# Optimization experiments

Hardware: AMD Instinct MI355X
Metric: run time of the kernel (lower is better)

The kernel has to match this reference:

```python
import jax, jax.numpy as jnp
import numpy as np

P = 512        # number of graph pairs
MAXN = 192     # max(len_s) by construction
D_IN = 32      # num_input_features
HID = 64       # hidden_dim
REG = 0.1      # entropic reg
ITERS = 8      # numItermax in forward call
DEG = 8        # avg degree for synthetic edges


def setup_inputs() -> dict:
    key = jax.random.key(0)
    ks = jax.random.split(key, 16)
    len_s = np.asarray(96 + (np.arange(P) % 97), dtype=np.int32)          # 96..192
    len_t = np.asarray(32 + ((np.arange(P) * 7) % 65), dtype=np.int32)    # 32..96 <= len_s
    Ns, Nt = int(len_s.sum()), int(len_t.sum())
    return {
        "x_s": jax.random.normal(ks[0], (Ns, D_IN), jnp.float32),
        "x_t": jax.random.normal(ks[1], (Nt, D_IN), jnp.float32),
        "W_rel0": 0.1 * jax.random.normal(ks[2], (D_IN, HID), jnp.float32),
        "b_rel0": 0.1 * jax.random.normal(ks[3], (HID,), jnp.float32),
        "W_root0": 0.1 * jax.random.normal(ks[4], (D_IN, HID), jnp.float32),
        "W_rel1": 0.1 * jax.random.normal(ks[5], (HID, HID), jnp.float32),
        "b_rel1": 0.1 * jax.random.normal(ks[6], (HID,), jnp.float32),
        "W_root1": 0.1 * jax.random.normal(ks[7], (HID, HID), jnp.float32),
        "W_e": 0.1 * jax.random.normal(ks[8], (D_IN + 2 * HID, 64), jnp.float32),
        "b_e": 0.1 * jax.random.normal(ks[9], (64,), jnp.float32),
        "virtual": jax.random.uniform(ks[10], (64,), jnp.float32),
        "edge_index_s": jax.random.randint(ks[11], (2, Ns * DEG), 0, Ns, dtype=jnp.int32),
        "edge_index_t": jax.random.randint(ks[12], (2, Nt * DEG), 0, Nt, dtype=jnp.int32),
        "len_s": jnp.asarray(len_s),
        "len_t": jnp.asarray(len_t),
    }


def _normalize(x):
    return x / jnp.clip(jnp.linalg.norm(x, axis=-1, keepdims=True), 1e-12)


def _gnn_embed(x, ei, layers, W_e, b_e):
    # GraphConv: out = lin_rel(sum_{j->i} x_j) + lin_root(x_i), then relu; cat all layer outputs
    outs = [x]
    h = x
    for (Wr, br, Wo) in layers:
        agg = jax.ops.segment_sum(h[ei[0]], ei[1], num_segments=h.shape[0])
        h = jax.nn.relu(agg @ Wr + br + h @ Wo)
        outs.append(h)
    emb = jnp.concatenate(outs, axis=1) @ W_e + b_e
    return _normalize(emb)


def _pad_gather(emb, lens):
    # [total, E] -> [P, MAXN, E] via per-pair offsets (indices clipped; invalid masked later)
    off = jnp.cumsum(lens) - lens
    idx = jnp.clip(off[:, None] + jnp.arange(MAXN)[None, :], 0, emb.shape[0] - 1)
    return emb[idx]


def reference(x_s, x_t, W_rel0, b_rel0, W_root0, W_rel1, b_rel1, W_root1,
              W_e, b_e, virtual, edge_index_s, edge_index_t, len_s, len_t):
    layers = [(W_rel0, b_rel0, W_root0), (W_rel1, b_rel1, W_root1)]
    emb_s = _gnn_embed(x_s, edge_index_s, layers, W_e, b_e)  # [Ns, 64]
    emb_t = _gnn_embed(x_t, edge_index_t, layers, W_e, b_e)  # [Nt, 64]
    virt = _normalize(virtual[None, :])[0]

    s_pad = _pad_gather(emb_s, len_s)  # [P, MAXN, 64]
    t_pad = _pad_gather(emb_t, len_t)  # [P, MAXN, 64]
    j = jnp.arange(MAXN)
    # columns >= len_t use the virtual node embedding (covers j in [m, n))
    t_mask = (j[None, :] < len_t[:, None])[:, :, None]
    t_aug = jnp.where(t_mask, t_pad, virt[None, None, :])

    # Euclidean cdist via quadratic expansion
    sq_s = jnp.sum(s_pad * s_pad, -1)                              # [P, MAXN]
    sq_t = jnp.sum(t_aug * t_aug, -1)                              # [P, MAXN]
    dot = jnp.einsum('pid,pjd->pij', s_pad, t_aug)                 # [P, MAXN, MAXN]
    cd = jnp.sqrt(jnp.maximum(sq_s[:, :, None] + sq_t[:, None, :] - 2.0 * dot, 1e-12))

    # padded cost: real block = cdist, bottom-right pad block = 0, rest = 1000
    row_valid = j[None, :] < len_s[:, None]                        # [P, MAXN] (n = len_s)
    in_block = row_valid[:, :, None] & row_valid[:, None, :]
    pad_block = (~row_valid)[:, :, None] & (~row_valid)[:, None, :]
    cost = jnp.where(in_block, cd, jnp.where(pad_block, 0.0, 1000.0))

    # Sinkhorn-Knopp, a = b = ones(MAXN) so Kp = K and updates are 1/(K v), 1/(K^T u)
    K = jnp.exp(-cost / REG)

    def body(_, uv):
        u, v = uv
        v = 1.0 / jnp.einsum('pij,pi->pj', K, u)
        u = 1.0 / jnp.einsum('pij,pj->pi', K, v)
        return (u, v)

    u0 = jnp.full((P, MAXN), 1.0 / MAXN, dtype=cost.dtype)
    u, v = jax.lax.fori_loop(0, ITERS, body, (u0, u0))
    gamma = jax.lax.stop_gradient(u[:, :, None] * K * v[:, None, :])

    geds = jnp.sum(gamma * cost, axis=(1, 2))
    geds2 = geds / (len_s + len_t).astype(cost.dtype)
    return gamma, cost, geds2
```

## Files before the change

### kernel.cpp

```cpp
#include <hip/hip_runtime.h>
#include <math.h>

#define PAIRS 512
#define MAXN 192

__global__ void offsets_kernel(const int* __restrict__ ls, const int* __restrict__ lt,
                               int* __restrict__ off) {
    __shared__ int wa[8], wb[8];
    int t = threadIdx.x;
    int a = ls[t], b = lt[t];
    int ia = a, ib = b;
#pragma unroll
    for (int d = 1; d < 64; d <<= 1) {
        int xa = __shfl_up(ia, d, 64);
        int xb = __shfl_up(ib, d, 64);
        if ((t & 63) >= d) { ia += xa; ib += xb; }
    }
    if ((t & 63) == 63) { wa[t >> 6] = ia; wb[t >> 6] = ib; }
    __syncthreads();
    int pa = 0, pb = 0;
    for (int w = 0; w < (t >> 6); w++) { pa += wa[w]; pb += wb[w]; }
    off[t] = pa + ia - a;
    off[PAIRS + t] = pb + ib - b;
}

__global__ __launch_bounds__(256) void count2_kernel(const int* __restrict__ eiS,
                                                     const int* __restrict__ eiT,
                                                     int* __restrict__ cnt,
                                                     int Es, int Et, int split) {
    int e = blockIdx.x * 256 + threadIdx.x;
    if (e < Es) atomicAdd(&cnt[eiS[Es + e]], 1);
    else if (e < Es + Et) atomicAdd(&cnt[split + eiT[Et + (e - Es)]], 1);
}

__global__ __launch_bounds__(256) void scan1_kernel(int* __restrict__ data,
                                                    int* __restrict__ blockSums, int N) {
    __shared__ int sc[256];
    int t = threadIdx.x;
    int base = blockIdx.x * 1024;
    int v[4];
    int s = 0;
#pragma unroll
    for (int q = 0; q < 4; q++) {
        int i = base + t * 4 + q;
        v[q] = (i < N) ? data[i] : 0;
        s += v[q];
    }
    sc[t] = s;
    __syncthreads();
    for (int d = 1; d < 256; d <<= 1) {
        int x = (t >= d) ? sc[t - d] : 0;
        __syncthreads();
        sc[t] += x;
        __syncthreads();
    }
    int excl = sc[t] - s;
#pragma unroll
    for (int q = 0; q < 4; q++) {
        int i = base + t * 4 + q;
        if (i < N) { data[i] = excl; excl += v[q]; }
    }
    if (t == 255) blockSums[blockIdx.x] = sc[255];
}

__global__ void scan2_kernel(int* __restrict__ blockSums, int B) {
    __shared__ int sh[256];
    int t = threadIdx.x;
    int v = (t < B) ? blockSums[t] : 0;
    sh[t] = v;
    __syncthreads();
    for (int d = 1; d < 256; d <<= 1) {
        int x = (t >= d) ? sh[t - d] : 0;
        __syncthreads();
        sh[t] += x;
        __syncthreads();
    }
    if (t < B) blockSums[t] = sh[t] - v;
}

__global__ __launch_bounds__(256) void scan3_kernel(int* __restrict__ data,
                                                    const int* __restrict__ blockSums,
                                                    int* __restrict__ cursor, int N) {
    int i = blockIdx.x * 256 + threadIdx.x;
    if (i < N) {
        int v = data[i] + blockSums[i >> 10];
        data[i] = v;
        cursor[i] = v;
    }
}

__global__ __launch_bounds__(256) void fill2_kernel(const int* __restrict__ eiS,
                                                    const int* __restrict__ eiT,
                                                    int* __restrict__ cursor,
                                                    int* __restrict__ src,
                                                    int Es, int Et, int split) {
    int e = blockIdx.x * 256 + threadIdx.x;
    if (e < Es) {
        int p = atomicAdd(&cursor[eiS[Es + e]], 1);
        src[p] = eiS[e];
    } else if (e < Es + Et) {
        int ee = e - Es;
        int p = atomicAdd(&cursor[split + eiT[Et + ee]], 1);
        src[p] = eiT[ee];
    }
}

template <int F>
__global__ __launch_bounds__(256) void gather_kernel(const float* __restrict__ featA,
                                                     const float* __restrict__ featB,
                                                     int split,
                                                     const int* __restrict__ rs,
                                                     const int* __restrict__ re,
                                                     const int* __restrict__ src,
                                                     float* __restrict__ agg, int N) {
    int gid = blockIdx.x * 256 + threadIdx.x;
    int row = gid / F;
    int lane = threadIdx.x & (F - 1);
    if (row >= N) return;
    int b = rs[row], e = re[row];
    int cnt = e - b;
    const float* feat = (row < split) ? featA : featB;
    int pre = cnt < F ? cnt : F;
    int sidx = (lane < cnt) ? src[b + lane] : 0;
    float acc = 0.f;
    for (int q = 0; q < pre; q++) {
        int s = __shfl(sidx, q, F);
        acc += feat[(size_t)s * F + lane];
    }
    for (int q = b + F; q < e; q++) acc += feat[(size_t)src[q] * F + lane];
    agg[(size_t)row * F + lane] = acc;
}


template <int KIN>
__global__ __launch_bounds__(256) void lin_gemm_kernel(const float* __restrict__ agg,
    const float* __restrict__ hinA, const float* __restrict__ hinB, int split,
    const float* __restrict__ Wrel, const float* __restrict__ brel,
    const float* __restrict__ Wroot, float* __restrict__ hout, int N) {
    __shared__ float Abuf[64 * 65];
    __shared__ float4 Wbuf[64 * 16];
    int tid = threadIdx.x;
    int i = tid & 15, j = tid >> 4;
    int rowbase = blockIdx.x * 64;
    float4 bv = ((const float4*)brel)[j];
    float acc[4][4];
#pragma unroll
    for (int r = 0; r < 4; r++) { acc[r][0] = bv.x; acc[r][1] = bv.y; acc[r][2] = bv.z; acc[r][3] = bv.w; }

    for (int c0 = 0; c0 < 2 * KIN; c0 += 64) {
        __syncthreads();
        for (int t = tid; t < 1024; t += 256) {
            int r = t >> 4, k4 = t & 15;
            int kg = c0 + 4 * k4;
            int row = rowbase + r; if (row >= N) row = N - 1;
            float4 v;
            if (kg < KIN) {
                v = ((const float4*)(agg + (size_t)row * KIN))[kg >> 2];
            } else {
                int kk = kg - KIN;
                const float* h = (row < split) ? hinA + (size_t)row * KIN
                                               : hinB + (size_t)(row - split) * KIN;
                v = ((const float4*)h)[kk >> 2];
            }
            float* d = Abuf + r * 65 + 4 * k4;
            d[0] = v.x; d[1] = v.y; d[2] = v.z; d[3] = v.w;
        }
        for (int t = tid; t < 1024; t += 256) {
            int k = t >> 4, jj = t & 15;
            int kg = c0 + k;
            const float* Wsrc = (kg < KIN) ? (Wrel + (size_t)kg * 64)
                                           : (Wroot + (size_t)(kg - KIN) * 64);
            Wbuf[t] = ((const float4*)Wsrc)[jj];
        }
        __syncthreads();
#pragma unroll 4
        for (int k = 0; k < 64; k++) {
            float4 wv = Wbuf[k * 16 + j];
            float a0 = Abuf[(4 * i + 0) * 65 + k];
            float a1 = Abuf[(4 * i + 1) * 65 + k];
            float a2 = Abuf[(4 * i + 2) * 65 + k];
            float a3 = Abuf[(4 * i + 3) * 65 + k];
            acc[0][0] = fmaf(a0, wv.x, acc[0][0]); acc[0][1] = fmaf(a0, wv.y, acc[0][1]);
            acc[0][2] = fmaf(a0, wv.z, acc[0][2]); acc[0][3] = fmaf(a0, wv.w, acc[0][3]);
            acc[1][0] = fmaf(a1, wv.x, acc[1][0]); acc[1][1] = fmaf(a1, wv.y, acc[1][1]);
            acc[1][2] = fmaf(a1, wv.z, acc[1][2]); acc[1][3] = fmaf(a1, wv.w, acc[1][3]);
            acc[2][0] = fmaf(a2, wv.x, acc[2][0]); acc[2][1] = fmaf(a2, wv.y, acc[2][1]);
            acc[2][2] = fmaf(a2, wv.z, acc[2][2]); acc[2][3] = fmaf(a2, wv.w, acc[2][3]);
            acc[3][0] = fmaf(a3, wv.x, acc[3][0]); acc[3][1] = fmaf(a3, wv.y, acc[3][1]);
            acc[3][2] = fmaf(a3, wv.z, acc[3][2]); acc[3][3] = fmaf(a3, wv.w, acc[3][3]);
        }
    }
#pragma unroll
    for (int r = 0; r < 4; r++) {
        int row = rowbase + 4 * i + r;
        if (row < N) {
            float4 o = make_float4(fmaxf(acc[r][0], 0.f), fmaxf(acc[r][1], 0.f),
                                   fmaxf(acc[r][2], 0.f), fmaxf(acc[r][3], 0.f));
            ((float4*)(hout + (size_t)row * 64))[j] = o;
        }
    }
}

__global__ __launch_bounds__(256) void emb_gemm_kernel(const float* __restrict__ xA,
    const float* __restrict__ xB, int split,
    const float* __restrict__ h1, const float* __restrict__ h2,
    const float* __restrict__ We, const float* __restrict__ be,
    float* __restrict__ emb, int N) {
    __shared__ float Abuf[64 * 65];
    __shared__ float4 Wbuf[64 * 16];
    int tid = threadIdx.x;
    int i = tid & 15, j = tid >> 4;
    int rowbase = blockIdx.x * 64;
    float4 bv = ((const float4*)be)[j];
    float acc[4][4];
#pragma unroll
    for (int r = 0; r < 4; r++) { acc[r][0] = bv.x; acc[r][1] = bv.y; acc[r][2] = bv.z; acc[r][3] = bv.w; }

    for (int c0 = 0; c0 < 160; c0 += 64) {
        int kw = (160 - c0 < 64) ? (160 - c0) : 64;
        int sh = (kw == 64) ? 4 : 3;
        int msk = (1 << sh) - 1;
        __syncthreads();
        for (int t = tid; t < 64 * (kw >> 2); t += 256) {
            int r = t >> sh, k4 = t & msk;
            int kg = c0 + 4 * k4;
            int row = rowbase + r; if (row >= N) row = N - 1;
            float4 v;
            if (kg < 32) {
                const float* x = (row < split) ? xA + (size_t)row * 32
                                               : xB + (size_t)(row - split) * 32;
                v = ((const float4*)x)[kg >> 2];
            } else if (kg < 96) {
                v = ((const float4*)(h1 + (size_t)row * 64))[(kg - 32) >> 2];
            } else {
                v = ((const float4*)(h2 + (size_t)row * 64))[(kg - 96) >> 2];
            }
            float* d = Abuf + r * 65 + 4 * k4;
            d[0] = v.x; d[1] = v.y; d[2] = v.z; d[3] = v.w;
        }
        for (int t = tid; t < kw * 16; t += 256) {
            int k = t >> 4, jj = t & 15;
            Wbuf[t] = ((const float4*)(We + (size_t)(c0 + k) * 64))[jj];
        }
        __syncthreads();
#pragma unroll 4
        for (int k = 0; k < kw; k++) {
            float4 wv = Wbuf[k * 16 + j];
            float a0 = Abuf[(4 * i + 0) * 65 + k];
            float a1 = Abuf[(4 * i + 1) * 65 + k];
            float a2 = Abuf[(4 * i + 2) * 65 + k];
            float a3 = Abuf[(4 * i + 3) * 65 + k];
            acc[0][0] = fmaf(a0, wv.x, acc[0][0]); acc[0][1] = fmaf(a0, wv.y, acc[0][1]);
            acc[0][2] = fmaf(a0, wv.z, acc[0][2]); acc[0][3] = fmaf(a0, wv.w, acc[0][3]);
            acc[1][0] = fmaf(a1, wv.x, acc[1][0]); acc[1][1] = fmaf(a1, wv.y, acc[1][1]);
            acc[1][2] = fmaf(a1, wv.z, acc[1][2]); acc[1][3] = fmaf(a1, wv.w, acc[1][3]);
            acc[2][0] = fmaf(a2, wv.x, acc[2][0]); acc[2][1] = fmaf(a2, wv.y, acc[2][1]);
            acc[2][2] = fmaf(a2, wv.z, acc[2][2]); acc[2][3] = fmaf(a2, wv.w, acc[2][3]);
            acc[3][0] = fmaf(a3, wv.x, acc[3][0]); acc[3][1] = fmaf(a3, wv.y, acc[3][1]);
            acc[3][2] = fmaf(a3, wv.z, acc[3][2]); acc[3][3] = fmaf(a3, wv.w, acc[3][3]);
        }
    }
    __syncthreads();
#pragma unroll
    for (int r = 0; r < 4; r++)
#pragma unroll
        for (int c = 0; c < 4; c++)
            Abuf[(4 * i + r) * 65 + 4 * j + c] = acc[r][c];
    __syncthreads();
    int lane = tid & 63, wv = tid >> 6;
    for (int rr = 0; rr < 16; rr++) {
        int r = wv * 16 + rr;
        float val = Abuf[r * 65 + lane];
        float ss = val * val;
#pragma unroll
        for (int d = 32; d > 0; d >>= 1) ss += __shfl_xor(ss, d, 64);
        int row = rowbase + r;
        if (row < N) emb[(size_t)row * 64 + lane] = val / fmaxf(sqrtf(ss), 1e-12f);
    }
}

__global__ __launch_bounds__(256) void cost_kernel(const float* __restrict__ embS,
                                                   const float* __restrict__ embT,
                                                   const float* __restrict__ vraw,
                                                   const int* __restrict__ lenS,
                                                   const int* __restrict__ lenT,
                                                   const int* __restrict__ off,
                                                   float* __restrict__ cost, int Ns) {
    int p = blockIdx.x >> 1;
    int half = blockIdx.x & 1;
    __shared__ float sS[96 * 65];
    __shared__ float sT[192 * 65];
    __shared__ float sqS[96];
    __shared__ float sqT[192];
    __shared__ __align__(16) float virt[64];
    int tid = threadIdx.x;
    int n = lenS[p], m = lenT[p];
    int offs = off[p], offt = off[PAIRS + p];

    if (tid < 64) {
        float v = vraw[tid];
        float ss = v * v;
#pragma unroll
        for (int d = 32; d > 0; d >>= 1) ss += __shfl_xor(ss, d, 64);
        virt[tid] = v / fmaxf(sqrtf(ss), 1e-12f);
    }
    __syncthreads();

    for (int t = tid; t < 96 * 16; t += 256) {
        int r = t >> 4, q = t & 15;
        int gi = offs + half * 96 + r;
        if (gi > Ns - 1) gi = Ns - 1;
        float4 vv = ((const float4*)embS)[(size_t)gi * 16 + q];
        sS[r * 65 + q * 4 + 0] = vv.x;
        sS[r * 65 + q * 4 + 1] = vv.y;
        sS[r * 65 + q * 4 + 2] = vv.z;
        sS[r * 65 + q * 4 + 3] = vv.w;
    }
    for (int t = tid; t < 192 * 16; t += 256) {
        int j = t >> 4, q = t & 15;
        float4 vv;
        if (j < m) vv = ((const float4*)embT)[(size_t)(offt + j) * 16 + q];
        else       vv = ((const float4*)virt)[q];
        sT[j * 65 + q * 4 + 0] = vv.x;
        sT[j * 65 + q * 4 + 1] = vv.y;
        sT[j * 65 + q * 4 + 2] = vv.z;
        sT[j * 65 + q * 4 + 3] = vv.w;
    }
    __syncthreads();

    for (int r = tid; r < 96; r += 256) {
        float s = 0.f;
#pragma unroll
        for (int k = 0; k < 64; k++) { float a = sS[r * 65 + k]; s = fmaf(a, a, s); }
        sqS[r] = s;
    }
    for (int j = tid; j < 192; j += 256) {
        float s = 0.f;
#pragma unroll
        for (int k = 0; k < 64; k++) { float a = sT[j * 65 + k]; s = fmaf(a, a, s); }
        sqT[j] = s;
    }
    __syncthreads();

    int ti = tid & 15, tj = tid >> 4;
    int ibase = ti * 6, jbase = tj * 12;
    float acc[6][12];
#pragma unroll
    for (int r = 0; r < 6; r++)
#pragma unroll
        for (int c = 0; c < 12; c++) acc[r][c] = 0.f;

    for (int k = 0; k < 64; k++) {
        float sv[6], tv[12];
#pragma unroll
        for (int r = 0; r < 6; r++) sv[r] = sS[(ibase + r) * 65 + k];
#pragma unroll
        for (int c = 0; c < 12; c++) tv[c] = sT[(jbase + c) * 65 + k];
#pragma unroll
        for (int r = 0; r < 6; r++)
#pragma unroll
            for (int c = 0; c < 12; c++) acc[r][c] = fmaf(sv[r], tv[c], acc[r][c]);
    }

    int i0 = half * 96;
#pragma unroll
    for (int r = 0; r < 6; r++) {
        int i = i0 + ibase + r;
        bool rv = i < n;
        float sqi = sqS[ibase + r];
        float* orow = cost + ((size_t)p * MAXN + i) * MAXN + jbase;
        float tmp[12];
#pragma unroll
        for (int c = 0; c < 12; c++) {
            int j = jbase + c;
            float cd = sqrtf(fmaxf(sqi + sqT[j] - 2.f * acc[r][c], 1e-12f));
            bool cv = j < n;
            tmp[c] = (rv && cv) ? cd : ((!rv && !cv) ? 0.f : 1000.f);
        }
#pragma unroll
        for (int q = 0; q < 3; q++)
            ((float4*)orow)[q] = make_float4(tmp[4 * q], tmp[4 * q + 1], tmp[4 * q + 2], tmp[4 * q + 3]);
    }
}

__global__ __launch_bounds__(1024) void sinkhorn_kernel(const float* __restrict__ cost,
                                                        float* __restrict__ gamma,
                                                        float* __restrict__ geds2,
                                                        const int* __restrict__ lenS,
                                                        const int* __restrict__ lenT) {
    int p = blockIdx.x;
    __shared__ float K[MAXN * 193];
    __shared__ float part[4 * MAXN];
    __shared__ float u[MAXN];
    __shared__ float v[MAXN];
    __shared__ float wsum[16];
    int tid = threadIdx.x;
    const float* cp = cost + (size_t)p * MAXN * MAXN;

    for (int t = tid; t < MAXN * MAXN; t += 1024) {
        int i = t / MAXN, j = t - i * MAXN;
        K[i * 193 + j] = expf(-10.f * cp[t]);
    }
    if (tid < MAXN) u[tid] = 1.f / 192.f;

    int g = tid >> 8;
    int r = tid & 255;
    int base = g * 48;

    for (int it = 0; it < 8; it++) {
        __syncthreads();
        if (r < MAXN) {
            float s = 0.f;
#pragma unroll
            for (int q = 0; q < 48; q++) { int i = base + q; s = fmaf(K[i * 193 + r], u[i], s); }
            part[g * MAXN + r] = s;
        }
        __syncthreads();
        if (tid < MAXN)
            v[tid] = 1.f / (part[tid] + part[MAXN + tid] + part[2 * MAXN + tid] + part[3 * MAXN + tid]);
        __syncthreads();
        if (r < MAXN) {
            float s = 0.f;
#pragma unroll
            for (int q = 0; q < 48; q++) { int j = base + q; s = fmaf(K[r * 193 + j], v[j], s); }
            part[g * MAXN + r] = s;
        }
        __syncthreads();
        if (tid < MAXN)
            u[tid] = 1.f / (part[tid] + part[MAXN + tid] + part[2 * MAXN + tid] + part[3 * MAXN + tid]);
    }
    __syncthreads();

    float acc = 0.f;
    float* gp = gamma + (size_t)p * MAXN * MAXN;
    for (int t = tid; t < MAXN * MAXN; t += 1024) {
        int i = t / MAXN, j = t - i * MAXN;
        float Kij = K[i * 193 + j];
        float gg = u[i] * Kij * v[j];
        gp[t] = gg;
        if (Kij > 0.f) acc = fmaf(gg, -0.1f * logf(Kij), acc);
    }
#pragma unroll
    for (int d = 32; d > 0; d >>= 1) acc += __shfl_xor(acc, d, 64);
    if ((tid & 63) == 0) wsum[tid >> 6] = acc;
    __syncthreads();
    if (tid == 0) {
        float s = 0.f;
        for (int q = 0; q < 16; q++) s += wsum[q];
        geds2[p] = s / (float)(lenS[p] + lenT[p]);
    }
}

extern "C" void kernel_launch(void* const* d_in, const int* in_sizes, int n_in,
                              void* d_out, int out_size, void* d_ws, size_t ws_size,
                              hipStream_t stream) {
    const float* x_s     = (const float*)d_in[0];
    const float* x_t     = (const float*)d_in[1];
    const float* W_rel0  = (const float*)d_in[2];
    const float* b_rel0  = (const float*)d_in[3];
    const float* W_root0 = (const float*)d_in[4];
    const float* W_rel1  = (const float*)d_in[5];
    const float* b_rel1  = (const float*)d_in[6];
    const float* W_root1 = (const float*)d_in[7];
    const float* W_e     = (const float*)d_in[8];
    const float* b_e     = (const float*)d_in[9];
    const float* virt    = (const float*)d_in[10];
    const int*   ei_s    = (const int*)d_in[11];
    const int*   ei_t    = (const int*)d_in[12];
    const int*   len_s   = (const int*)d_in[13];
    const int*   len_t   = (const int*)d_in[14];

    int Ns = in_sizes[0] / 32;
    int Nt = in_sizes[1] / 32;
    int Es = in_sizes[11] / 2;
    int Et = in_sizes[12] / 2;
    int Ntot = Ns + Nt;
    int Etot = Es + Et;

    char* w = (char*)d_ws;
    int* off  = (int*)w;              w += 1024 * 4;
    int* bsum = (int*)w;              w += 256 * 4;
    int* rs   = (int*)w;              w += (size_t)Ntot * 4;
    int* cur  = (int*)w;              w += (size_t)Ntot * 4;
    int* src  = (int*)w;              w += (size_t)Etot * 4;
    w = (char*)(((size_t)w + 255) & ~(size_t)255);
    float* agg = (float*)w;           w += (size_t)Ntot * 64 * 4;
    float* h1  = (float*)w;           w += (size_t)Ntot * 64 * 4;
    float* h2  = (float*)w;           w += (size_t)Ntot * 64 * 4;

    float* out_gamma = (float*)d_out;
    float* out_cost  = out_gamma + (size_t)PAIRS * MAXN * MAXN;
    float* out_geds  = out_cost + (size_t)PAIRS * MAXN * MAXN;

    offsets_kernel<<<1, PAIRS, 0, stream>>>(len_s, len_t, off);

    hipMemsetAsync(rs, 0, (size_t)Ntot * 4, stream);
    count2_kernel<<<(Etot + 255) / 256, 256, 0, stream>>>(ei_s, ei_t, rs, Es, Et, Ns);
    int nb = (Ntot + 1023) / 1024;
    scan1_kernel<<<nb, 256, 0, stream>>>(rs, bsum, Ntot);
    scan2_kernel<<<1, 256, 0, stream>>>(bsum, nb);
    scan3_kernel<<<(Ntot + 255) / 256, 256, 0, stream>>>(rs, bsum, cur, Ntot);
    fill2_kernel<<<(Etot + 255) / 256, 256, 0, stream>>>(ei_s, ei_t, cur, src, Es, Et, Ns);

    int gblk = (Ntot + 63) / 64;

    gather_kernel<32><<<(int)(((long long)Ntot * 32 + 255) / 256), 256, 0, stream>>>(
        x_s, x_t, Ns, rs, cur, src, agg, Ntot);
    lin_gemm_kernel<32><<<gblk, 256, 0, stream>>>(
        agg, x_s, x_t, Ns, W_rel0, b_rel0, W_root0, h1, Ntot);
    gather_kernel<64><<<(int)(((long long)Ntot * 64 + 255) / 256), 256, 0, stream>>>(
        h1, h1, Ns, rs, cur, src, agg, Ntot);
    lin_gemm_kernel<64><<<gblk, 256, 0, stream>>>(
        agg, h1, h1, Ntot + 1, W_rel1, b_rel1, W_root1, h2, Ntot);
    emb_gemm_kernel<<<gblk, 256, 0, stream>>>(
        x_s, x_t, Ns, h1, h2, W_e, b_e, agg, Ntot);

    cost_kernel<<<PAIRS * 2, 256, 0, stream>>>(
        agg, agg + (size_t)Ns * 64, virt, len_s, len_t, off, out_cost, Ns);
    sinkhorn_kernel<<<PAIRS, 1024, 0, stream>>>(out_cost, out_gamma, out_geds, len_s, len_t);
}
```

Before: 612.2 us.

## Fuse cost and Sinkhorn into one register-resident kernel and single-block scan

Merges the cost-matrix kernel and the Sinkhorn kernel into one block per pair. Each thread keeps a 6x6 tile of the cost and then of K in registers, and the row and column reductions go through a shared partial-sum buffer. This removes the global round trip of the cost matrix and the separate exp pass. The CSR prefix scan is also collapsed from three launches into one 1024-thread kernel. The second gather now passes the target-side h1 offset, which changes indexing for target rows. In exchange, occupancy drops to one large block per CU, with heavy LDS use and high register pressure.

```diff
diff --git a/kernel.cpp b/kernel.cpp
--- a/kernel.cpp
+++ b/kernel.cpp
@@ -33,59 +33,31 @@
     else if (e < Es + Et) atomicAdd(&cnt[split + eiT[Et + (e - Es)]], 1);
 }
 
-__global__ __launch_bounds__(256) void scan1_kernel(int* __restrict__ data,
-                                                    int* __restrict__ blockSums, int N) {
-    __shared__ int sc[256];
+__global__ __launch_bounds__(1024) void scan_all_kernel(int* __restrict__ data,
+                                                        int* __restrict__ cursor, int N) {
+    __shared__ int wsums[16];
     int t = threadIdx.x;
-    int base = blockIdx.x * 1024;
-    int v[4];
+    int per = (N + 1023) >> 10;
+    int lo = t * per; if (lo > N) lo = N;
+    int hi = lo + per; if (hi > N) hi = N;
     int s = 0;
-#pragma unroll
-    for (int q = 0; q < 4; q++) {
-        int i = base + t * 4 + q;
-        v[q] = (i < N) ? data[i] : 0;
-        s += v[q];
-    }
-    sc[t] = s;
-    __syncthreads();
-    for (int d = 1; d < 256; d <<= 1) {
-        int x = (t >= d) ? sc[t - d] : 0;
-        __syncthreads();
-        sc[t] += x;
-        __syncthreads();
-    }
-    int excl = sc[t] - s;
-#pragma unroll
-    for (int q = 0; q < 4; q++) {
-        int i = base + t * 4 + q;
-        if (i < N) { data[i] = excl; excl += v[q]; }
-    }
-    if (t == 255) blockSums[blockIdx.x] = sc[255];
-}
-
-__global__ void scan2_kernel(int* __restrict__ blockSums, int B) {
-    __shared__ int sh[256];
-    int t = threadIdx.x;
-    int v = (t < B) ? blockSums[t] : 0;
-    sh[t] = v;
-    __syncthreads();
-    for (int d = 1; d < 256; d <<= 1) {
-        int x = (t >= d) ? sh[t - d] : 0;
-        __syncthreads();
-        sh[t] += x;
-        __syncthreads();
-    }
-    if (t < B) blockSums[t] = sh[t] - v;
-}
-
-__global__ __launch_bounds__(256) void scan3_kernel(int* __restrict__ data,
-                                                    const int* __restrict__ blockSums,
-                                                    int* __restrict__ cursor, int N) {
-    int i = blockIdx.x * 256 + threadIdx.x;
-    if (i < N) {
-        int v = data[i] + blockSums[i >> 10];
-        data[i] = v;
-        cursor[i] = v;
+    for (int i = lo; i < hi; i++) s += data[i];
+    int inc = s;
+#pragma unroll
+    for (int d = 1; d < 64; d <<= 1) {
+        int x = __shfl_up(inc, d, 64);
+        if ((t & 63) >= d) inc += x;
+    }
+    if ((t & 63) == 63) wsums[t >> 6] = inc;
+    __syncthreads();
+    int base = 0;
+    for (int q = 0; q < (t >> 6); q++) base += wsums[q];
+    int excl = base + inc - s;
+    for (int i = lo; i < hi; i++) {
+        int v = data[i];
+        data[i] = excl;
+        cursor[i] = excl;
+        excl += v;
     }
 }
 
@@ -131,7 +103,6 @@
     agg[(size_t)row * F + lane] = acc;
 }
 
-
 template <int KIN>
 __global__ __launch_bounds__(256) void lin_gemm_kernel(const float* __restrict__ agg,
     const float* __restrict__ hinA, const float* __restrict__ hinB, int split,
@@ -279,62 +250,66 @@
     }
 }
 
-__global__ __launch_bounds__(256) void cost_kernel(const float* __restrict__ embS,
-                                                   const float* __restrict__ embT,
-                                                   const float* __restrict__ vraw,
-                                                   const int* __restrict__ lenS,
-                                                   const int* __restrict__ lenT,
-                                                   const int* __restrict__ off,
-                                                   float* __restrict__ cost, int Ns) {
-    int p = blockIdx.x >> 1;
-    int half = blockIdx.x & 1;
-    __shared__ float sS[96 * 65];
-    __shared__ float sT[192 * 65];
-    __shared__ float sqS[96];
-    __shared__ float sqT[192];
+__global__ __launch_bounds__(1024, 1) void cost_sink_kernel(const float* __restrict__ embS,
+                                                            const float* __restrict__ embT,
+                                                            const float* __restrict__ vraw,
+                                                            const int* __restrict__ lenS,
+                                                            const int* __restrict__ lenT,
+                                                            const int* __restrict__ off,
+                                                            float* __restrict__ cost,
+                                                            float* __restrict__ gamma,
+                                                            float* __restrict__ geds2,
+                                                            int Ns) {
+    __shared__ float sST[24960];
+    __shared__ float part[32 * 193];
+    __shared__ float u[MAXN];
+    __shared__ float v[MAXN];
+    __shared__ float sqS[MAXN];
+    __shared__ float sqT[MAXN];
     __shared__ __align__(16) float virt[64];
+    __shared__ float wsum[16];
+
+    int p = blockIdx.x;
     int tid = threadIdx.x;
+    int ti = tid & 31, tj = tid >> 5;
     int n = lenS[p], m = lenT[p];
     int offs = off[p], offt = off[PAIRS + p];
+    float* sS = sST;
+    float* sT = sST + 12480;
 
     if (tid < 64) {
-        float v = vraw[tid];
-        float ss = v * v;
+        float vv = vraw[tid];
+        float ss = vv * vv;
 #pragma unroll
         for (int d = 32; d > 0; d >>= 1) ss += __shfl_xor(ss, d, 64);
-        virt[tid] = v / fmaxf(sqrtf(ss), 1e-12f);
-    }
-    __syncthreads();
-
-    for (int t = tid; t < 96 * 16; t += 256) {
+        virt[tid] = vv / fmaxf(sqrtf(ss), 1e-12f);
+    }
+    __syncthreads();
+
+    for (int t = tid; t < 192 * 16; t += 1024) {
         int r = t >> 4, q = t & 15;
-        int gi = offs + half * 96 + r;
-        if (gi > Ns - 1) gi = Ns - 1;
+        int gi = offs + r; if (gi > Ns - 1) gi = Ns - 1;
         float4 vv = ((const float4*)embS)[(size_t)gi * 16 + q];
-        sS[r * 65 + q * 4 + 0] = vv.x;
-        sS[r * 65 + q * 4 + 1] = vv.y;
-        sS[r * 65 + q * 4 + 2] = vv.z;
-        sS[r * 65 + q * 4 + 3] = vv.w;
-    }
-    for (int t = tid; t < 192 * 16; t += 256) {
+        float* d = sS + r * 65 + q * 4;
+        d[0] = vv.x; d[1] = vv.y; d[2] = vv.z; d[3] = vv.w;
+    }
+    for (int t = tid; t < 192 * 16; t += 1024) {
         int j = t >> 4, q = t & 15;
         float4 vv;
         if (j < m) vv = ((const float4*)embT)[(size_t)(offt + j) * 16 + q];
         else       vv = ((const float4*)virt)[q];
-        sT[j * 65 + q * 4 + 0] = vv.x;
-        sT[j * 65 + q * 4 + 1] = vv.y;
-        sT[j * 65 + q * 4 + 2] = vv.z;
-        sT[j * 65 + q * 4 + 3] = vv.w;
-    }
-    __syncthreads();
-
-    for (int r = tid; r < 96; r += 256) {
+        float* d = sT + j * 65 + q * 4;
+        d[0] = vv.x; d[1] = vv.y; d[2] = vv.z; d[3] = vv.w;
+    }
+    __syncthreads();
+
+    if (tid < 192) {
         float s = 0.f;
 #pragma unroll
-        for (int k = 0; k < 64; k++) { float a = sS[r * 65 + k]; s = fmaf(a, a, s); }
-        sqS[r] = s;
-    }
-    for (int j = tid; j < 192; j += 256) {
+        for (int k = 0; k < 64; k++) { float a = sS[tid * 65 + k]; s = fmaf(a, a, s); }
+        sqS[tid] = s;
+    } else if (tid < 384) {
+        int j = tid - 192;
         float s = 0.f;
 #pragma unroll
         for (int k = 0; k < 64; k++) { float a = sT[j * 65 + k]; s = fmaf(a, a, s); }
@@ -342,112 +317,150 @@
     }
     __syncthreads();
 
-    int ti = tid & 15, tj = tid >> 4;
-    int ibase = ti * 6, jbase = tj * 12;
-    float acc[6][12];
+    float kt[6][6];
 #pragma unroll
     for (int r = 0; r < 6; r++)
 #pragma unroll
-        for (int c = 0; c < 12; c++) acc[r][c] = 0.f;
-
+        for (int c = 0; c < 6; c++) kt[r][c] = 0.f;
+
+    int ib = ti * 6, jb = tj * 6;
     for (int k = 0; k < 64; k++) {
-        float sv[6], tv[12];
-#pragma unroll
-        for (int r = 0; r < 6; r++) sv[r] = sS[(ibase + r) * 65 + k];
-#pragma unroll
-        for (int c = 0; c < 12; c++) tv[c] = sT[(jbase + c) * 65 + k];
+        float sv[6], tv[6];
+#pragma unroll
+        for (int r = 0; r < 6; r++) sv[r] = sS[(ib + r) * 65 + k];
+#pragma unroll
+        for (int c = 0; c < 6; c++) tv[c] = sT[(jb + c) * 65 + k];
 #pragma unroll
         for (int r = 0; r < 6; r++)
 #pragma unroll
-            for (int c = 0; c < 12; c++) acc[r][c] = fmaf(sv[r], tv[c], acc[r][c]);
-    }
-
-    int i0 = half * 96;
+            for (int c = 0; c < 6; c++) kt[r][c] = fmaf(sv[r], tv[c], kt[r][c]);
+    }
 #pragma unroll
     for (int r = 0; r < 6; r++) {
-        int i = i0 + ibase + r;
+        int i = ib + r;
         bool rv = i < n;
-        float sqi = sqS[ibase + r];
-        float* orow = cost + ((size_t)p * MAXN + i) * MAXN + jbase;
-        float tmp[12];
-#pragma unroll
-        for (int c = 0; c < 12; c++) {
-            int j = jbase + c;
-            float cd = sqrtf(fmaxf(sqi + sqT[j] - 2.f * acc[r][c], 1e-12f));
+        float sqi = sqS[i];
+#pragma unroll
+        for (int c = 0; c < 6; c++) {
+            int j = jb + c;
+            float cd = sqrtf(fmaxf(sqi + sqT[j] - 2.f * kt[r][c], 1e-12f));
             bool cv = j < n;
-            tmp[c] = (rv && cv) ? cd : ((!rv && !cv) ? 0.f : 1000.f);
-        }
-#pragma unroll
-        for (int q = 0; q < 3; q++)
-            ((float4*)orow)[q] = make_float4(tmp[4 * q], tmp[4 * q + 1], tmp[4 * q + 2], tmp[4 * q + 3]);
-    }
-}
-
-__global__ __launch_bounds__(1024) void sinkhorn_kernel(const float* __restrict__ cost,
-                                                        float* __restrict__ gamma,
-                                                        float* __restrict__ geds2,
-                                                        const int* __restrict__ lenS,
-                                                        const int* __restrict__ lenT) {
-    int p = blockIdx.x;
-    __shared__ float K[MAXN * 193];
-    __shared__ float part[4 * MAXN];
-    __shared__ float u[MAXN];
-    __shared__ float v[MAXN];
-    __shared__ float wsum[16];
-    int tid = threadIdx.x;
-    const float* cp = cost + (size_t)p * MAXN * MAXN;
-
-    for (int t = tid; t < MAXN * MAXN; t += 1024) {
-        int i = t / MAXN, j = t - i * MAXN;
-        K[i * 193 + j] = expf(-10.f * cp[t]);
-    }
+            kt[r][c] = (rv && cv) ? cd : ((!rv && !cv) ? 0.f : 1000.f);
+        }
+    }
+
+    float* bounce = sST;
+    float* cp = cost + (size_t)p * MAXN * MAXN;
+    for (int h = 0; h < 2; h++) {
+        __syncthreads();
+        if ((ti >> 4) == h) {
+            int rb = ib - 96 * h;
+#pragma unroll
+            for (int r = 0; r < 6; r++)
+#pragma unroll
+                for (int c = 0; c < 6; c++)
+                    bounce[(rb + r) * 193 + jb + c] = kt[r][c];
+        }
+        __syncthreads();
+        for (int q = 0; q < 18; q++) {
+            int el = q * 1024 + tid;
+            int row = el / 192, col = el - row * 192;
+            cp[(size_t)(96 * h + row) * 192 + col] = bounce[row * 193 + col];
+        }
+    }
+
+#pragma unroll
+    for (int r = 0; r < 6; r++)
+#pragma unroll
+        for (int c = 0; c < 6; c++) kt[r][c] = expf(-10.f * kt[r][c]);
+
     if (tid < MAXN) u[tid] = 1.f / 192.f;
 
-    int g = tid >> 8;
-    int r = tid & 255;
-    int base = g * 48;
-
     for (int it = 0; it < 8; it++) {
         __syncthreads();
-        if (r < MAXN) {
+        {
+            float ur[6];
+#pragma unroll
+            for (int r = 0; r < 6; r++) ur[r] = u[ib + r];
+#pragma unroll
+            for (int c = 0; c < 6; c++) {
+                float s = 0.f;
+#pragma unroll
+                for (int r = 0; r < 6; r++) s = fmaf(kt[r][c], ur[r], s);
+                part[ti * 193 + jb + c] = s;
+            }
+        }
+        __syncthreads();
+        if (tid < MAXN) {
             float s = 0.f;
 #pragma unroll
-            for (int q = 0; q < 48; q++) { int i = base + q; s = fmaf(K[i * 193 + r], u[i], s); }
-            part[g * MAXN + r] = s;
-        }
-        __syncthreads();
-        if (tid < MAXN)
-            v[tid] = 1.f / (part[tid] + part[MAXN + tid] + part[2 * MAXN + tid] + part[3 * MAXN + tid]);
-        __syncthreads();
-        if (r < MAXN) {
+            for (int q = 0; q < 32; q++) s += part[q * 193 + tid];
+            v[tid] = 1.f / s;
+        }
+        __syncthreads();
+        {
+            float vc[6];
+#pragma unroll
+            for (int c = 0; c < 6; c++) vc[c] = v[jb + c];
+#pragma unroll
+            for (int r = 0; r < 6; r++) {
+                float s = 0.f;
+#pragma unroll
+                for (int c = 0; c < 6; c++) s = fmaf(kt[r][c], vc[c], s);
+                part[tj * 193 + ib + r] = s;
+            }
+        }
+        __syncthreads();
+        if (tid < MAXN) {
             float s = 0.f;
 #pragma unroll
-            for (int q = 0; q < 48; q++) { int j = base + q; s = fmaf(K[r * 193 + j], v[j], s); }
-            part[g * MAXN + r] = s;
-        }
-        __syncthreads();
-        if (tid < MAXN)
-            u[tid] = 1.f / (part[tid] + part[MAXN + tid] + part[2 * MAXN + tid] + part[3 * MAXN + tid]);
-    }
-    __syncthreads();
+            for (int q = 0; q < 32; q++) s += part[q * 193 + tid];
+            u[tid] = 1.f / s;
+        }
+    }
+    __syncthreads();
+
+    float ur[6], vc[6];
+#pragma unroll
+    for (int r = 0; r < 6; r++) ur[r] = u[ib + r];
+#pragma unroll
+    for (int c = 0; c < 6; c++) vc[c] = v[jb + c];
 
     float acc = 0.f;
-    float* gp = gamma + (size_t)p * MAXN * MAXN;
-    for (int t = tid; t < MAXN * MAXN; t += 1024) {
-        int i = t / MAXN, j = t - i * MAXN;
-        float Kij = K[i * 193 + j];
-        float gg = u[i] * Kij * v[j];
-        gp[t] = gg;
-        if (Kij > 0.f) acc = fmaf(gg, -0.1f * logf(Kij), acc);
-    }
+#pragma unroll
+    for (int r = 0; r < 6; r++)
+#pragma unroll
+        for (int c = 0; c < 6; c++) {
+            float kk = kt[r][c];
+            float g = ur[r] * kk * vc[c];
+            if (kk > 0.f) acc = fmaf(g, -0.1f * logf(kk), acc);
+        }
 #pragma unroll
     for (int d = 32; d > 0; d >>= 1) acc += __shfl_xor(acc, d, 64);
     if ((tid & 63) == 0) wsum[tid >> 6] = acc;
-    __syncthreads();
+
+    float* gp = gamma + (size_t)p * MAXN * MAXN;
+    for (int h = 0; h < 2; h++) {
+        __syncthreads();
+        if ((ti >> 4) == h) {
+            int rb = ib - 96 * h;
+#pragma unroll
+            for (int r = 0; r < 6; r++)
+#pragma unroll
+                for (int c = 0; c < 6; c++)
+                    bounce[(rb + r) * 193 + jb + c] = ur[r] * kt[r][c] * vc[c];
+        }
+        __syncthreads();
+        for (int q = 0; q < 18; q++) {
+            int el = q * 1024 + tid;
+            int row = el / 192, col = el - row * 192;
+            gp[(size_t)(96 * h + row) * 192 + col] = bounce[row * 193 + col];
+        }
+    }
     if (tid == 0) {
         float s = 0.f;
         for (int q = 0; q < 16; q++) s += wsum[q];
-        geds2[p] = s / (float)(lenS[p] + lenT[p]);
+        geds2[p] = s / (float)(n + m);
     }
 }
 
@@ -479,7 +492,6 @@
 
     char* w = (char*)d_ws;
     int* off  = (int*)w;              w += 1024 * 4;
-    int* bsum = (int*)w;              w += 256 * 4;
     int* rs   = (int*)w;              w += (size_t)Ntot * 4;
     int* cur  = (int*)w;              w += (size_t)Ntot * 4;
     int* src  = (int*)w;              w += (size_t)Etot * 4;
@@ -496,10 +508,7 @@
 
     hipMemsetAsync(rs, 0, (size_t)Ntot * 4, stream);
     count2_kernel<<<(Etot + 255) / 256, 256, 0, stream>>>(ei_s, ei_t, rs, Es, Et, Ns);
-    int nb = (Ntot + 1023) / 1024;
-    scan1_kernel<<<nb, 256, 0, stream>>>(rs, bsum, Ntot);
-    scan2_kernel<<<1, 256, 0, stream>>>(bsum, nb);
-    scan3_kernel<<<(Ntot + 255) / 256, 256, 0, stream>>>(rs, bsum, cur, Ntot);
+    scan_all_kernel<<<1, 1024, 0, stream>>>(rs, cur, Ntot);
     fill2_kernel<<<(Etot + 255) / 256, 256, 0, stream>>>(ei_s, ei_t, cur, src, Es, Et, Ns);
 
     int gblk = (Ntot + 63) / 64;
@@ -509,13 +518,13 @@
     lin_gemm_kernel<32><<<gblk, 256, 0, stream>>>(
         agg, x_s, x_t, Ns, W_rel0, b_rel0, W_root0, h1, Ntot);
     gather_kernel<64><<<(int)(((long long)Ntot * 64 + 255) / 256), 256, 0, stream>>>(
-        h1, h1, Ns, rs, cur, src, agg, Ntot);
+        h1, h1 + (size_t)Ns * 64, Ns, rs, cur, src, agg, Ntot);
     lin_gemm_kernel<64><<<gblk, 256, 0, stream>>>(
         agg, h1, h1, Ntot + 1, W_rel1, b_rel1, W_root1, h2, Ntot);
     emb_gemm_kernel<<<gblk, 256, 0, stream>>>(
         x_s, x_t, Ns, h1, h2, W_e, b_e, agg, Ntot);
 
-    cost_kernel<<<PAIRS * 2, 256, 0, stream>>>(
-        agg, agg + (size_t)Ns * 64, virt, len_s, len_t, off, out_cost, Ns);
-    sinkhorn_kernel<<<PAIRS, 1024, 0, stream>>>(out_cost, out_gamma, out_geds, len_s, len_t);
-}
+    cost_sink_kernel<<<PAIRS, 1024, 0, stream>>>(
+        agg, agg + (size_t)Ns * 64, virt, len_s, len_t, off,
+        out_cost, out_gamma, out_geds, Ns);
+}
```

New measurement: 876.3 us. +43.1%, slower.
